# Optimization experiments

Measured on AMD Instinct MI355X. Metric: run time of the kernel, lower is better.

The kernel has to match this reference:

```python
import jax, jax.numpy as jnp
import numpy as np

INPUT_SIZE = 20
HIDDEN = 51
OUT = 1
B = 4096
T = 512


def _init_lstm_params(key, in_dim, hid_dim):
    # PyTorch LSTMCell init: U(-1/sqrt(hid), 1/sqrt(hid))
    k = 1.0 / np.sqrt(hid_dim)
    ks = jax.random.split(key, 4)
    W_ih = jax.random.uniform(ks[0], (4 * hid_dim, in_dim), minval=-k, maxval=k, dtype=jnp.float32)
    W_hh = jax.random.uniform(ks[1], (4 * hid_dim, hid_dim), minval=-k, maxval=k, dtype=jnp.float32)
    b_ih = jax.random.uniform(ks[2], (4 * hid_dim,), minval=-k, maxval=k, dtype=jnp.float32)
    b_hh = jax.random.uniform(ks[3], (4 * hid_dim,), minval=-k, maxval=k, dtype=jnp.float32)
    return W_ih, W_hh, b_ih, b_hh


def setup_inputs() -> dict:
    key = jax.random.key(0)
    k_x, k1, k2, k3, k4 = jax.random.split(key, 5)
    x = jax.random.normal(k_x, (B, T, INPUT_SIZE), dtype=jnp.float32)
    W_ih1, W_hh1, b_ih1, b_hh1 = _init_lstm_params(k1, INPUT_SIZE, HIDDEN)
    W_ih2, W_hh2, b_ih2, b_hh2 = _init_lstm_params(k2, HIDDEN, OUT)
    kl = 1.0 / np.sqrt(OUT)
    ka, kb, kc, kd = jax.random.split(k3, 4)
    W_mu = jax.random.uniform(ka, (OUT, OUT), minval=-kl, maxval=kl, dtype=jnp.float32)
    b_mu = jax.random.uniform(kb, (OUT,), minval=-kl, maxval=kl, dtype=jnp.float32)
    W_lv = jax.random.uniform(kc, (OUT, OUT), minval=-kl, maxval=kl, dtype=jnp.float32)
    b_lv = jax.random.uniform(kd, (OUT,), minval=-kl, maxval=kl, dtype=jnp.float32)
    return {
        "x": x,
        "W_ih1": W_ih1, "W_hh1": W_hh1, "b_ih1": b_ih1, "b_hh1": b_hh1,
        "W_ih2": W_ih2, "W_hh2": W_hh2, "b_ih2": b_ih2, "b_hh2": b_hh2,
        "W_mu": W_mu, "b_mu": b_mu, "W_lv": W_lv, "b_lv": b_lv,
    }


def _lstm_cell(x_t, h, c, W_ih, W_hh, b_ih, b_hh):
    # PyTorch LSTMCell: gate order i, f, g, o
    gates = x_t @ W_ih.T + b_ih + h @ W_hh.T + b_hh
    i, f, g, o = jnp.split(gates, 4, axis=-1)
    c_new = jax.nn.sigmoid(f) * c + jax.nn.sigmoid(i) * jnp.tanh(g)
    h_new = jax.nn.sigmoid(o) * jnp.tanh(c_new)
    return h_new, c_new


def reference(x, W_ih1, W_hh1, b_ih1, b_hh1, W_ih2, W_hh2, b_ih2, b_hh2, W_mu, b_mu, W_lv, b_lv):
    bsz = x.shape[0]
    h1 = jnp.zeros((bsz, HIDDEN), dtype=x.dtype)
    c1 = jnp.zeros((bsz, HIDDEN), dtype=x.dtype)
    h2 = jnp.zeros((bsz, OUT), dtype=x.dtype)
    c2 = jnp.zeros((bsz, OUT), dtype=x.dtype)

    def step(carry, x_t):
        h1, c1, h2, c2 = carry
        h1, c1 = _lstm_cell(x_t, h1, c1, W_ih1, W_hh1, b_ih1, b_hh1)
        h2, c2 = _lstm_cell(h1, h2, c2, W_ih2, W_hh2, b_ih2, b_hh2)
        return (h1, c1, h2, c2), h2

    xs = jnp.swapaxes(x, 0, 1)  # [T, B, input_size]
    _, h2_seq = jax.lax.scan(step, (h1, c1, h2, c2), xs)  # h2_seq: [T, B, 1]
    agg = jnp.mean(h2_seq, axis=0)  # [B, 1] mean over time
    mu = agg @ W_mu.T + b_mu
    log_var = agg @ W_lv.T + b_lv
    sigma = jnp.exp(0.5 * log_var)
    lower = mu - 1.96 * sigma
    upper = mu + 1.96 * sigma
    return (lower, mu, upper, log_var)
```

## Files before the change

### kernel.cpp

```cpp
#include <hip/hip_runtime.h>

#define B_TOT 4096
#define T_STEPS 512
#define IN 20
#define HID 51

typedef float f32x4 __attribute__((ext_vector_type(4)));
typedef short s16x8 __attribute__((ext_vector_type(8)));

__device__ __forceinline__ unsigned short f2bf(float f) {
    unsigned int u = __float_as_uint(f);
    unsigned int r = (u + 0x7fffu + ((u >> 16) & 1u)) >> 16;
    return (unsigned short)r;
}

__device__ __forceinline__ float fast_rcp(float x) { return __builtin_amdgcn_rcpf(x); }
__device__ __forceinline__ float sigf(float x) { return fast_rcp(1.0f + __expf(-x)); }
__device__ __forceinline__ float tanh_(float x) { return 1.0f - 2.0f * fast_rcp(1.0f + __expf(2.0f * x)); }


__global__ __launch_bounds__(256, 1)
void lstm_fused(const float* __restrict__ x,
                const float* __restrict__ Wih1, const float* __restrict__ Whh1,
                const float* __restrict__ bih1, const float* __restrict__ bhh1,
                const float* __restrict__ Wih2, const float* __restrict__ Whh2,
                const float* __restrict__ bih2, const float* __restrict__ bhh2,
                const float* __restrict__ Wmu,  const float* __restrict__ bmu,
                const float* __restrict__ Wlv,  const float* __restrict__ blv,
                float* __restrict__ out)
{
    __shared__ __align__(16) unsigned short vA[2][3][64][8];

    const int tid  = threadIdx.x;
    const int lane = tid & 63;
    const int w    = tid >> 6;
    const int bidx = blockIdx.x;

    const int tbase = (w < 3) ? 3 * w : 9;
    const int ntile = (w < 3) ? 3 : 4;
    const bool isST = (w == 0);
    const bool isL2 = (w == 2);

    s16x8 wfrag[4][3];
    f32x4 binit[4];
    #pragma unroll
    for (int ti = 0; ti < 4; ++ti) {
        const int tau = tbase + ti;
        const int m = lane & 15;
        const bool act = (ti < ntile);
        #pragma unroll
        for (int ks = 0; ks < 3; ++ks) {
            s16x8 f;
            #pragma unroll
            for (int j = 0; j < 8; ++j) {
                int k = ks * 32 + ((lane >> 4) << 3) + j;
                float v = 0.0f;
                if (act) {
                    int g = m & 3, unit = tau * 4 + (m >> 2);
                    if (unit < HID) {
                        int row = g * HID + unit;
                        if (k < IN) v = Wih1[row * IN + k];
                        else if (k >= 32 && k < 32 + HID) v = Whh1[row * HID + (k - 32)];
                    }
                }
                f[j] = (short)f2bf(v);
            }
            wfrag[ti][ks] = f;
        }
        f32x4 bi = {0.f, 0.f, 0.f, 0.f};
        if (act) {
            int unit = tau * 4 + (lane >> 4);
            if (unit < HID) {
                #pragma unroll
                for (int r = 0; r < 4; ++r) bi[r] = bih1[r * HID + unit] + bhh1[r * HID + unit];
            }
        }
        binit[ti] = bi;
    }

    s16x8 l2frag[2];
    f32x4 l2binit = {0.f, 0.f, 0.f, 0.f};
    float whh2g[4];
    if (isL2) {
        const int m = lane & 15;
        #pragma unroll
        for (int ks = 1; ks < 3; ++ks) {
            s16x8 f;
            #pragma unroll
            for (int j = 0; j < 8; ++j) {
                int k = ks * 32 + ((lane >> 4) << 3) + j;
                float v = 0.0f;
                if (m < 4 && k >= 32 && k < 32 + HID) v = Wih2[m * HID + (k - 32)];
                f[j] = (short)f2bf(v);
            }
            l2frag[ks - 1] = f;
        }
        #pragma unroll
        for (int r = 0; r < 4; ++r) { whh2g[r] = Whh2[r]; l2binit[r] = bih2[r] + bhh2[r]; }
    }

    const float* sp[5];
    int srow[5], sj[5];
    if (isST) {
        #pragma unroll
        for (int i = 0; i < 5; ++i) {
            int e = i * 64 + lane;
            int b = e / IN, m = e % IN;
            sp[i]   = x + ((size_t)(bidx * 16 + b) * T_STEPS) * IN + m;
            srow[i] = ((m >> 3) & 3) * 16 + b;
            sj[i]   = m & 7;
        }
    }

    {
        unsigned short* vz = &vA[0][0][0][0];
        for (int i = tid; i < 2 * 3 * 64 * 8; i += 256) vz[i] = 0;
    }
    __syncthreads();
    float xr[5];
    if (isST) {
        #pragma unroll
        for (int i = 0; i < 5; ++i) {
            vA[0][0][srow[i]][sj[i]] = f2bf(sp[i][0]);
            xr[i] = sp[i][IN];
        }
    }
    __syncthreads();

    float c1[4] = {0.f, 0.f, 0.f, 0.f};
    float c2p = 0.f, h2p = 0.f, sum2 = 0.f;

    for (int t = 0; t < T_STEPS; ++t) {
        const int p  = t & 1;
        const int pn = p ^ 1;

        s16x8 bf0 = *(const s16x8*)&vA[p][0][lane][0];
        s16x8 bf1 = *(const s16x8*)&vA[p][1][lane][0];
        s16x8 bf2 = *(const s16x8*)&vA[p][2][lane][0];

        #pragma unroll
        for (int ti = 0; ti < 4; ++ti) {
            if (ti < ntile) {
                f32x4 a = binit[ti];
                a = __builtin_amdgcn_mfma_f32_16x16x32_bf16(wfrag[ti][0], bf0, a, 0, 0, 0);
                a = __builtin_amdgcn_mfma_f32_16x16x32_bf16(wfrag[ti][1], bf1, a, 0, 0, 0);
                a = __builtin_amdgcn_mfma_f32_16x16x32_bf16(wfrag[ti][2], bf2, a, 0, 0, 0);

                float c = sigf(a[1]) * c1[ti] + sigf(a[0]) * tanh_(a[2]);
                c1[ti] = c;
                float h = sigf(a[3]) * tanh_(c);
                int unit = (tbase + ti) * 4 + (lane >> 4);
                int k    = 32 + unit;
                int b    = lane & 15;
                vA[pn][k >> 5][(((k >> 3) & 3) << 4) + b][k & 7] = f2bf(h);
            }
        }

        if (isL2) {
            f32x4 a = l2binit;
            a = __builtin_amdgcn_mfma_f32_16x16x32_bf16(l2frag[0], bf1, a, 0, 0, 0);
            a = __builtin_amdgcn_mfma_f32_16x16x32_bf16(l2frag[1], bf2, a, 0, 0, 0);
            if (t > 0 && lane < 16) {
                float pi = a[0] + whh2g[0] * h2p;
                float pf = a[1] + whh2g[1] * h2p;
                float pg = a[2] + whh2g[2] * h2p;
                float po = a[3] + whh2g[3] * h2p;
                float c2 = sigf(pf) * c2p + sigf(pi) * tanh_(pg);
                c2p = c2;
                h2p = sigf(po) * tanh_(c2);
                sum2 += h2p;
            }
        }

        if (isST) {
            const int t2 = (t < T_STEPS - 2) ? t + 2 : T_STEPS - 1;
            #pragma unroll
            for (int i = 0; i < 5; ++i) {
                vA[pn][0][srow[i]][sj[i]] = f2bf(xr[i]);
                xr[i] = sp[i][(size_t)t2 * IN];
            }
        }

        __syncthreads();
    }

    if (isL2) {
        s16x8 bf1 = *(const s16x8*)&vA[0][1][lane][0];
        s16x8 bf2 = *(const s16x8*)&vA[0][2][lane][0];
        f32x4 a = l2binit;
        a = __builtin_amdgcn_mfma_f32_16x16x32_bf16(l2frag[0], bf1, a, 0, 0, 0);
        a = __builtin_amdgcn_mfma_f32_16x16x32_bf16(l2frag[1], bf2, a, 0, 0, 0);
        if (lane < 16) {
            float pi = a[0] + whh2g[0] * h2p;
            float pf = a[1] + whh2g[1] * h2p;
            float pg = a[2] + whh2g[2] * h2p;
            float po = a[3] + whh2g[3] * h2p;
            float c2 = sigf(pf) * c2p + sigf(pi) * tanh_(pg);
            h2p = sigf(po) * tanh_(c2);
            sum2 += h2p;

            float agg = sum2 * (1.0f / 512.0f);
            float mu  = Wmu[0] * agg + bmu[0];
            float lv  = Wlv[0] * agg + blv[0];
            float sg  = __expf(0.5f * lv);
            int bg = bidx * 16 + lane;
            out[bg]             = mu - 1.96f * sg;
            out[B_TOT + bg]     = mu;
            out[2 * B_TOT + bg] = mu + 1.96f * sg;
            out[3 * B_TOT + bg] = lv;
        }
    }
}

extern "C" void kernel_launch(void* const* d_in, const int* in_sizes, int n_in,
                              void* d_out, int out_size, void* d_ws, size_t ws_size,
                              hipStream_t stream) {
    const float* x    = (const float*)d_in[0];
    const float* Wih1 = (const float*)d_in[1];
    const float* Whh1 = (const float*)d_in[2];
    const float* bih1 = (const float*)d_in[3];
    const float* bhh1 = (const float*)d_in[4];
    const float* Wih2 = (const float*)d_in[5];
    const float* Whh2 = (const float*)d_in[6];
    const float* bih2 = (const float*)d_in[7];
    const float* bhh2 = (const float*)d_in[8];
    const float* Wmu  = (const float*)d_in[9];
    const float* bmu  = (const float*)d_in[10];
    const float* Wlv  = (const float*)d_in[11];
    const float* blv  = (const float*)d_in[12];
    float* out = (float*)d_out;

    lstm_fused<<<dim3(B_TOT / 16), dim3(256), 0, stream>>>(
        x, Wih1, Whh1, bih1, bhh1, Wih2, Whh2, bih2, bhh2, Wmu, bmu, Wlv, blv, out);
}
```

Measured before the change: 502.9 us.

## Balance LSTM tiles across waves and fold layer-2 cell into a shared MFMA tile

Redistributes the 13 layer-1 hidden tiles plus the layer-2 gate computation so every wave runs exactly four MFMA tiles, packing the layer-2 gates into the spare rows of the last partial tile. It also splits the per-step x staging loads between two waves and interleaves the MFMA chains and activation math across tiles for more instruction-level parallelism. The aim is to remove the load imbalance that made one wave the critical path each step. In exchange, every wave now does a full four tiles and uniform activation math, including masked lanes.

```diff
diff --git a/kernel.cpp b/kernel.cpp
--- a/kernel.cpp
+++ b/kernel.cpp
@@ -10,13 +10,9 @@
 
 __device__ __forceinline__ unsigned short f2bf(float f) {
     unsigned int u = __float_as_uint(f);
-    unsigned int r = (u + 0x7fffu + ((u >> 16) & 1u)) >> 16;
-    return (unsigned short)r;
+    return (unsigned short)((u + 0x7fffu + ((u >> 16) & 1u)) >> 16);
 }
-
 __device__ __forceinline__ float fast_rcp(float x) { return __builtin_amdgcn_rcpf(x); }
-__device__ __forceinline__ float sigf(float x) { return fast_rcp(1.0f + __expf(-x)); }
-__device__ __forceinline__ float tanh_(float x) { return 1.0f - 2.0f * fast_rcp(1.0f + __expf(2.0f * x)); }
 
 
 __global__ __launch_bounds__(256, 1)
@@ -34,29 +30,40 @@
     const int tid  = threadIdx.x;
     const int lane = tid & 63;
     const int w    = tid >> 6;
+    const int q    = lane >> 4;
+    const int m    = lane & 15;
     const int bidx = blockIdx.x;
 
-    const int tbase = (w < 3) ? 3 * w : 9;
-    const int ntile = (w < 3) ? 3 : 4;
-    const bool isST = (w == 0);
-    const bool isL2 = (w == 2);
-
-    s16x8 wfrag[4][3];
+    int tau[4];
+    {
+        int base = 3 * w + (w >= 2 ? 1 : 0);
+        tau[0] = base; tau[1] = base + 1; tau[2] = base + 2;
+        tau[3] = (w == 1) ? 6 : ((w == 0) ? 13 : ((w == 2) ? 14 : 15));
+    }
+
+    s16x8 wf[4][3];
     f32x4 binit[4];
     #pragma unroll
-    for (int ti = 0; ti < 4; ++ti) {
-        const int tau = tbase + ti;
-        const int m = lane & 15;
-        const bool act = (ti < ntile);
+    for (int s = 0; s < 4; ++s) {
+        const int t = tau[s];
         #pragma unroll
         for (int ks = 0; ks < 3; ++ks) {
             s16x8 f;
             #pragma unroll
             for (int j = 0; j < 8; ++j) {
-                int k = ks * 32 + ((lane >> 4) << 3) + j;
+                int k = ks * 32 + (q << 3) + j;
                 float v = 0.0f;
-                if (act) {
-                    int g = m & 3, unit = tau * 4 + (m >> 2);
+                if (t == 12) {
+                    if (m < 4) {
+                        if (k >= 32 && k < 32 + HID) v = Wih2[m * HID + (k - 32)];
+                    } else {
+                        int unit = 47 + (m >> 2), g = m & 3;
+                        int row = g * HID + unit;
+                        if (k < IN) v = Wih1[row * IN + k];
+                        else if (k >= 32 && k < 32 + HID) v = Whh1[row * HID + (k - 32)];
+                    }
+                } else {
+                    int unit = t * 4 + (m >> 2), g = m & 3;
                     if (unit < HID) {
                         int row = g * HID + unit;
                         if (k < IN) v = Wih1[row * IN + k];
@@ -65,51 +72,55 @@
                 }
                 f[j] = (short)f2bf(v);
             }
-            wfrag[ti][ks] = f;
+            wf[s][ks] = f;
         }
         f32x4 bi = {0.f, 0.f, 0.f, 0.f};
-        if (act) {
-            int unit = tau * 4 + (lane >> 4);
+        if (t == 12) {
+            if (q == 0) {
+                #pragma unroll
+                for (int r = 0; r < 4; ++r) bi[r] = bih2[r] + bhh2[r];
+            } else {
+                int unit = 47 + q;
+                #pragma unroll
+                for (int r = 0; r < 4; ++r) bi[r] = bih1[r * HID + unit] + bhh1[r * HID + unit];
+            }
+        } else {
+            int unit = t * 4 + q;
             if (unit < HID) {
                 #pragma unroll
                 for (int r = 0; r < 4; ++r) bi[r] = bih1[r * HID + unit] + bhh1[r * HID + unit];
             }
         }
-        binit[ti] = bi;
-    }
-
-    s16x8 l2frag[2];
-    f32x4 l2binit = {0.f, 0.f, 0.f, 0.f};
-    float whh2g[4];
-    if (isL2) {
-        const int m = lane & 15;
-        #pragma unroll
-        for (int ks = 1; ks < 3; ++ks) {
-            s16x8 f;
-            #pragma unroll
-            for (int j = 0; j < 8; ++j) {
-                int k = ks * 32 + ((lane >> 4) << 3) + j;
-                float v = 0.0f;
-                if (m < 4 && k >= 32 && k < 32 + HID) v = Wih2[m * HID + (k - 32)];
-                f[j] = (short)f2bf(v);
-            }
-            l2frag[ks - 1] = f;
-        }
-        #pragma unroll
-        for (int r = 0; r < 4; ++r) { whh2g[r] = Whh2[r]; l2binit[r] = bih2[r] + bhh2[r]; }
-    }
-
-    const float* sp[5];
-    int srow[5], sj[5];
-    if (isST) {
-        #pragma unroll
-        for (int i = 0; i < 5; ++i) {
-            int e = i * 64 + lane;
-            int b = e / IN, m = e % IN;
-            sp[i]   = x + ((size_t)(bidx * 16 + b) * T_STEPS) * IN + m;
-            srow[i] = ((m >> 3) & 3) * 16 + b;
-            sj[i]   = m & 7;
-        }
+        binit[s] = bi;
+    }
+
+    const bool l2lane = (w == 3) && (q == 0);
+    const float msk = l2lane ? 1.f : 0.f;
+    float wadj[4];
+    #pragma unroll
+    for (int r = 0; r < 4; ++r) wadj[r] = l2lane ? Whh2[r] : 0.f;
+
+    int wch[4], wrow[4], wjj[4];
+    #pragma unroll
+    for (int s = 0; s < 4; ++s) {
+        int t = tau[s];
+        int u = (t == 12) ? ((q == 0) ? 51 : 47 + q) : t * 4 + q;
+        int k = 32 + u;
+        wch[s] = k >> 5; wrow[s] = (((k >> 3) & 3) << 4) + m; wjj[s] = k & 7;
+    }
+
+    const int ns = (w == 0) ? 3 : ((w == 2) ? 2 : 0);
+    const int ebase = (w == 2) ? 192 : 0;
+    const float* sp[3]; int srow[3], sj[3];
+    #pragma unroll
+    for (int i = 0; i < 3; ++i) {
+        if (i < ns) {
+            int e = ebase + i * 64 + lane;
+            int b = e / IN, mm = e % IN;
+            sp[i]   = x + ((size_t)(bidx * 16 + b) * T_STEPS) * IN + mm;
+            srow[i] = ((mm >> 3) & 3) * 16 + b;
+            sj[i]   = mm & 7;
+        } else { sp[i] = x; srow[i] = 0; sj[i] = 0; }
     }
 
     {
@@ -117,18 +128,16 @@
         for (int i = tid; i < 2 * 3 * 64 * 8; i += 256) vz[i] = 0;
     }
     __syncthreads();
-    float xr[5];
-    if (isST) {
-        #pragma unroll
-        for (int i = 0; i < 5; ++i) {
-            vA[0][0][srow[i]][sj[i]] = f2bf(sp[i][0]);
-            xr[i] = sp[i][IN];
-        }
+    float xr[3] = {0.f, 0.f, 0.f};
+    #pragma unroll
+    for (int i = 0; i < 3; ++i) if (i < ns) {
+        vA[0][0][srow[i]][sj[i]] = f2bf(sp[i][0]);
+        xr[i] = sp[i][IN];
     }
     __syncthreads();
 
     float c1[4] = {0.f, 0.f, 0.f, 0.f};
-    float c2p = 0.f, h2p = 0.f, sum2 = 0.f;
+    float hm = 0.f, sum2 = 0.f;
 
     for (int t = 0; t < T_STEPS; ++t) {
         const int p  = t & 1;
@@ -138,44 +147,69 @@
         s16x8 bf1 = *(const s16x8*)&vA[p][1][lane][0];
         s16x8 bf2 = *(const s16x8*)&vA[p][2][lane][0];
 
-        #pragma unroll
-        for (int ti = 0; ti < 4; ++ti) {
-            if (ti < ntile) {
-                f32x4 a = binit[ti];
-                a = __builtin_amdgcn_mfma_f32_16x16x32_bf16(wfrag[ti][0], bf0, a, 0, 0, 0);
-                a = __builtin_amdgcn_mfma_f32_16x16x32_bf16(wfrag[ti][1], bf1, a, 0, 0, 0);
-                a = __builtin_amdgcn_mfma_f32_16x16x32_bf16(wfrag[ti][2], bf2, a, 0, 0, 0);
-
-                float c = sigf(a[1]) * c1[ti] + sigf(a[0]) * tanh_(a[2]);
-                c1[ti] = c;
-                float h = sigf(a[3]) * tanh_(c);
-                int unit = (tbase + ti) * 4 + (lane >> 4);
-                int k    = 32 + unit;
-                int b    = lane & 15;
-                vA[pn][k >> 5][(((k >> 3) & 3) << 4) + b][k & 7] = f2bf(h);
-            }
-        }
-
-        if (isL2) {
-            f32x4 a = l2binit;
-            a = __builtin_amdgcn_mfma_f32_16x16x32_bf16(l2frag[0], bf1, a, 0, 0, 0);
-            a = __builtin_amdgcn_mfma_f32_16x16x32_bf16(l2frag[1], bf2, a, 0, 0, 0);
-            if (t > 0 && lane < 16) {
-                float pi = a[0] + whh2g[0] * h2p;
-                float pf = a[1] + whh2g[1] * h2p;
-                float pg = a[2] + whh2g[2] * h2p;
-                float po = a[3] + whh2g[3] * h2p;
-                float c2 = sigf(pf) * c2p + sigf(pi) * tanh_(pg);
-                c2p = c2;
-                h2p = sigf(po) * tanh_(c2);
-                sum2 += h2p;
-            }
-        }
-
-        if (isST) {
+        f32x4 acc[4];
+        #pragma unroll
+        for (int s = 0; s < 4; ++s) acc[s] = binit[s];
+        #pragma unroll
+        for (int r = 0; r < 4; ++r) acc[2][r] += wadj[r] * hm;
+
+        #pragma unroll
+        for (int s = 0; s < 4; ++s) acc[s] = __builtin_amdgcn_mfma_f32_16x16x32_bf16(wf[s][0], bf0, acc[s], 0, 0, 0);
+        #pragma unroll
+        for (int s = 0; s < 4; ++s) acc[s] = __builtin_amdgcn_mfma_f32_16x16x32_bf16(wf[s][1], bf1, acc[s], 0, 0, 0);
+        #pragma unroll
+        for (int s = 0; s < 4; ++s) acc[s] = __builtin_amdgcn_mfma_f32_16x16x32_bf16(wf[s][2], bf2, acc[s], 0, 0, 0);
+
+        float ei[4], ef[4], eg[4], eo[4];
+        #pragma unroll
+        for (int s = 0; s < 4; ++s) ei[s] = __expf(-acc[s][0]);
+        #pragma unroll
+        for (int s = 0; s < 4; ++s) ef[s] = __expf(-acc[s][1]);
+        #pragma unroll
+        for (int s = 0; s < 4; ++s) eg[s] = __expf(2.f * acc[s][2]);
+        #pragma unroll
+        for (int s = 0; s < 4; ++s) eo[s] = __expf(-acc[s][3]);
+        float ri[4], rf[4], rg[4], ro[4];
+        #pragma unroll
+        for (int s = 0; s < 4; ++s) ri[s] = fast_rcp(1.f + ei[s]);
+        #pragma unroll
+        for (int s = 0; s < 4; ++s) rf[s] = fast_rcp(1.f + ef[s]);
+        #pragma unroll
+        for (int s = 0; s < 4; ++s) rg[s] = fast_rcp(1.f + eg[s]);
+        #pragma unroll
+        for (int s = 0; s < 4; ++s) ro[s] = fast_rcp(1.f + eo[s]);
+        #pragma unroll
+        for (int s = 0; s < 4; ++s) {
+            float tg = fmaf(-2.f, rg[s], 1.f);
+            float pp = ri[s] * tg;
+            c1[s] = fmaf(rf[s], c1[s], pp);
+        }
+        float ey[4], ry[4], h[4];
+        #pragma unroll
+        for (int s = 0; s < 4; ++s) ey[s] = __expf(2.f * c1[s]);
+        #pragma unroll
+        for (int s = 0; s < 4; ++s) ry[s] = fast_rcp(1.f + ey[s]);
+        #pragma unroll
+        for (int s = 0; s < 4; ++s) {
+            float th = fmaf(-2.f, ry[s], 1.f);
+            h[s] = ro[s] * th;
+        }
+
+        hm   = h[2];
+        sum2 = fmaf(msk, h[2], sum2);
+        if (t == 0) {
+            if (l2lane) c1[2] = 0.f;
+            hm = 0.f; sum2 = 0.f;
+        }
+
+        #pragma unroll
+        for (int s = 0; s < 4; ++s)
+            vA[pn][wch[s]][wrow[s]][wjj[s]] = f2bf(h[s]);
+
+        if (ns) {
             const int t2 = (t < T_STEPS - 2) ? t + 2 : T_STEPS - 1;
             #pragma unroll
-            for (int i = 0; i < 5; ++i) {
+            for (int i = 0; i < 3; ++i) if (i < ns) {
                 vA[pn][0][srow[i]][sj[i]] = f2bf(xr[i]);
                 xr[i] = sp[i][(size_t)t2 * IN];
             }
@@ -184,20 +218,22 @@
         __syncthreads();
     }
 
-    if (isL2) {
+    if (w == 3) {
         s16x8 bf1 = *(const s16x8*)&vA[0][1][lane][0];
         s16x8 bf2 = *(const s16x8*)&vA[0][2][lane][0];
-        f32x4 a = l2binit;
-        a = __builtin_amdgcn_mfma_f32_16x16x32_bf16(l2frag[0], bf1, a, 0, 0, 0);
-        a = __builtin_amdgcn_mfma_f32_16x16x32_bf16(l2frag[1], bf2, a, 0, 0, 0);
+        f32x4 a = binit[2];
+        #pragma unroll
+        for (int r = 0; r < 4; ++r) a[r] += wadj[r] * hm;
+        a = __builtin_amdgcn_mfma_f32_16x16x32_bf16(wf[2][1], bf1, a, 0, 0, 0);
+        a = __builtin_amdgcn_mfma_f32_16x16x32_bf16(wf[2][2], bf2, a, 0, 0, 0);
         if (lane < 16) {
-            float pi = a[0] + whh2g[0] * h2p;
-            float pf = a[1] + whh2g[1] * h2p;
-            float pg = a[2] + whh2g[2] * h2p;
-            float po = a[3] + whh2g[3] * h2p;
-            float c2 = sigf(pf) * c2p + sigf(pi) * tanh_(pg);
-            h2p = sigf(po) * tanh_(c2);
-            sum2 += h2p;
+            float si = fast_rcp(1.f + __expf(-a[0]));
+            float sf = fast_rcp(1.f + __expf(-a[1]));
+            float tg = fmaf(-2.f, fast_rcp(1.f + __expf(2.f * a[2])), 1.f);
+            float so = fast_rcp(1.f + __expf(-a[3]));
+            float c2 = sf * c1[2] + si * tg;
+            float h2 = so * fmaf(-2.f, fast_rcp(1.f + __expf(2.f * c2)), 1.f);
+            sum2 += h2;
 
             float agg = sum2 * (1.0f / 512.0f);
             float mu  = Wmu[0] * agg + bmu[0];
```

After: 516.9 us. +2.8%, slower.
